# Optimization experiments

Hardware: AMD Instinct MI355X
Metric: run time of the kernel (lower is better)

The kernel has to match this reference:

```python
import jax, jax.numpy as jnp
import numpy as np

N_NODES = 150000
N_EDGES = 2400000
F_IN, HID, N_CLS = 22, 32, 6
BN_EPS = 1e-5


def setup_inputs() -> dict:
    key = jax.random.key(0)
    ks = jax.random.split(key, 10)
    x = jax.random.normal(ks[0], (N_NODES, F_IN), dtype=jnp.float32)
    edge_index = jax.random.randint(ks[1], (2, N_EDGES), 0, N_NODES, dtype=jnp.int64)
    # xavier-uniform style linear weights, zero biases (as in _init_weights)
    def xavier(k, fan_in, fan_out):
        lim = float(np.sqrt(6.0 / (fan_in + fan_out)))
        return jax.random.uniform(k, (fan_in, fan_out), jnp.float32, -lim, lim)
    return {
        "x": x,
        "edge_index": edge_index,
        "W_emb": xavier(ks[2], F_IN, HID),
        "b_emb": jnp.zeros((HID,), jnp.float32),
        "W_gcn": xavier(ks[3], HID, HID),
        "b_gcn": jnp.zeros((HID,), jnp.float32),
        "gamma": jnp.ones((HID,), jnp.float32),
        "beta": jnp.zeros((HID,), jnp.float32),
        "W_cls": xavier(ks[4], HID, N_CLS),
        "b_cls": jnp.zeros((N_CLS,), jnp.float32),
    }


def reference(x, edge_index, W_emb, b_emb, W_gcn, b_gcn, gamma, beta, W_cls, b_cls):
    N = x.shape[0]
    # embedding + relu
    h = jax.nn.relu(x @ W_emb + b_emb)                      # [N, HID]
    # GCNConv: linear transform first
    h = h @ W_gcn                                           # [N, HID]
    # add self-loops
    loops = jnp.arange(N, dtype=edge_index.dtype)
    src = jnp.concatenate([edge_index[0], loops])           # [E+N]
    dst = jnp.concatenate([edge_index[1], loops])
    # symmetric normalization deg^{-1/2} A_hat deg^{-1/2}
    deg = jax.ops.segment_sum(jnp.ones_like(dst, dtype=h.dtype), dst, num_segments=N)
    dis = jnp.where(deg > 0, jax.lax.rsqrt(jnp.where(deg > 0, deg, 1.0)), 0.0)
    norm = dis[src] * dis[dst]                              # [E+N]
    msg = h[src] * norm[:, None]                            # gather + scale
    agg = jax.ops.segment_sum(msg, dst, num_segments=N) + b_gcn
    # BatchNorm1d (training-mode batch statistics, biased variance)
    mean = jnp.mean(agg, axis=0)
    var = jnp.mean((agg - mean) ** 2, axis=0)
    hn = (agg - mean) * jax.lax.rsqrt(var + BN_EPS) * gamma + beta
    hn = jax.nn.relu(hn)
    # dropout is identity in eval; classifier
    return hn @ W_cls + b_cls
```

## Files before the change

kernel.cpp:

```cpp
#include <hip/hip_runtime.h>

#define N_NODES 150000
#define N_EDGES 2400000
#define F_IN    22
#define HID     32
#define N_CLS   6
#define BN_EPS  1e-5f

#define BSHIFT  8
#define BMASK   255
#define NB      ((N_NODES + BMASK) >> BSHIFT)
#define NBLK_BIN 256
#define CHUNK   ((N_EDGES + NBLK_BIN - 1) / NBLK_BIN)
#define CHUNK_H 8192
#define NBLK_H  ((N_EDGES + CHUNK_H - 1) / CHUNK_H)
#define NBLK_EMB ((N_NODES + 255) / 256)
#define NREP    8

__device__ __forceinline__ unsigned bf16rne(float f) {
    unsigned u = __float_as_uint(f);
    return (u + 0x7FFFu + ((u >> 16) & 1u)) >> 16;
}
__device__ __forceinline__ float bflo(unsigned p) { return __uint_as_float(p << 16); }
__device__ __forceinline__ float bfhi(unsigned p) { return __uint_as_float(p & 0xFFFF0000u); }

__global__ void embed_hist_kernel(const float* __restrict__ x,
                                  const float* __restrict__ W_emb,
                                  const float* __restrict__ b_emb,
                                  const float* __restrict__ W_gcn,
                                  unsigned* __restrict__ hb,
                                  const int* __restrict__ dst,
                                  int* __restrict__ bcnt) {
    if (blockIdx.x < NBLK_EMB) {
        __shared__ float sWe[F_IN * HID];
        __shared__ float sbe[HID];
        __shared__ float sWg[HID * HID];
        __shared__ unsigned sp[256 * 17];
        for (int t = threadIdx.x; t < F_IN * HID; t += blockDim.x) sWe[t] = W_emb[t];
        if (threadIdx.x < HID) sbe[threadIdx.x] = b_emb[threadIdx.x];
        for (int t = threadIdx.x; t < HID * HID; t += blockDim.x) sWg[t] = W_gcn[t];
        __syncthreads();

        int i = blockIdx.x * blockDim.x + threadIdx.x;
        bool act = i < N_NODES;

        if (act) {
            float xi[F_IN];
#pragma unroll
            for (int f = 0; f < F_IN; ++f) xi[f] = x[(size_t)i * F_IN + f];

            float h1[HID];
#pragma unroll
            for (int j = 0; j < HID; ++j) {
                float acc = sbe[j];
#pragma unroll
                for (int f = 0; f < F_IN; ++f) acc = fmaf(xi[f], sWe[f * HID + j], acc);
                h1[j] = fmaxf(acc, 0.0f);
            }
#pragma unroll
            for (int jj = 0; jj < HID / 2; ++jj) {
                float a0 = 0.0f, a1 = 0.0f;
#pragma unroll
                for (int f = 0; f < HID; ++f) {
                    a0 = fmaf(h1[f], sWg[f * HID + 2 * jj], a0);
                    a1 = fmaf(h1[f], sWg[f * HID + 2 * jj + 1], a1);
                }
                sp[threadIdx.x * 17 + jj] = bf16rne(a0) | (bf16rne(a1) << 16);
            }
        }
        __syncthreads();

        int nvalid = N_NODES - blockIdx.x * 256;
        if (nvalid > 256) nvalid = 256;
        int total = nvalid * 16;
        size_t gbase = (size_t)blockIdx.x * 256 * 16;
        for (int L = threadIdx.x; L < total; L += 256)
            hb[gbase + L] = sp[(L >> 4) * 17 + (L & 15)];
    } else {
        __shared__ int hloc[NB];
        for (int t = threadIdx.x; t < NB; t += 256) hloc[t] = 0;
        __syncthreads();
        int base = (blockIdx.x - NBLK_EMB) * CHUNK_H;
        int end = base + CHUNK_H; if (end > N_EDGES) end = N_EDGES;
        for (int i = base + threadIdx.x; i < end; i += 256)
            atomicAdd(&hloc[dst[i] >> BSHIFT], 1);
        __syncthreads();
        for (int t = threadIdx.x; t < NB; t += 256)
            if (hloc[t]) atomicAdd(&bcnt[t], hloc[t]);
    }
}

__global__ void bucket_scan_kernel(const int* __restrict__ bcnt,
                                   int* __restrict__ boff,
                                   int* __restrict__ bcur) {
    __shared__ int s[1024];
    int t = threadIdx.x;
    int v0 = (t < NB) ? bcnt[t] : 0;
    s[t] = v0;
    __syncthreads();
#pragma unroll
    for (int o = 1; o < 1024; o <<= 1) {
        int v = (t >= o) ? s[t - o] : 0;
        __syncthreads();
        s[t] += v;
        __syncthreads();
    }
    if (t < NB) {
        int e = s[t] - v0;
        boff[t] = e;
        bcur[t] = e;
    }
    if (t == NB - 1) boff[NB] = s[t];
}

__global__ void bin_edges_kernel(const int* __restrict__ src,
                                 const int* __restrict__ dst,
                                 int* __restrict__ bcur,
                                 unsigned int* __restrict__ binned) {
    __shared__ int hloc[NB];
    __shared__ int base[NB];
    __shared__ int lcur[NB];
    for (int t = threadIdx.x; t < NB; t += 512) hloc[t] = 0;
    __syncthreads();

    int cbase = blockIdx.x * CHUNK;
    int cend = cbase + CHUNK; if (cend > N_EDGES) cend = N_EDGES;
    for (int i = cbase + threadIdx.x; i < cend; i += 512)
        atomicAdd(&hloc[dst[i] >> BSHIFT], 1);
    __syncthreads();
    for (int t = threadIdx.x; t < NB; t += 512) {
        int c = hloc[t];
        base[t] = c ? atomicAdd(&bcur[t], c) : 0;
        lcur[t] = 0;
    }
    __syncthreads();
    for (int i = cbase + threadIdx.x; i < cend; i += 512) {
        int d = dst[i];
        int b = d >> BSHIFT;
        int r = atomicAdd(&lcur[b], 1);
        binned[base[b] + r] = ((unsigned)(d & BMASK) << 24) | (unsigned)src[i];
    }
}

__global__ void bucket_csr_kernel(const int* __restrict__ boff,
                                  const unsigned int* __restrict__ binned,
                                  int* __restrict__ sorted_src,
                                  int* __restrict__ off,
                                  float* __restrict__ dis) {
    __shared__ int s_cnt[256];
    __shared__ int s_scan[256];
    __shared__ int s_cur[256];
    int b = blockIdx.x;
    int t = threadIdx.x;
    int s0 = boff[b], s1 = boff[b + 1];
    int nbase = b << BSHIFT;
    int nnode = N_NODES - nbase; if (nnode > 256) nnode = 256;

    s_cnt[t] = 0;
    __syncthreads();
    for (int k = s0 + t; k < s1; k += 256)
        atomicAdd(&s_cnt[binned[k] >> 24], 1);
    __syncthreads();

    int v = s_cnt[t];
    s_scan[t] = v;
    __syncthreads();
#pragma unroll
    for (int o = 1; o < 256; o <<= 1) {
        int u = (t >= o) ? s_scan[t - o] : 0;
        __syncthreads();
        s_scan[t] += u;
        __syncthreads();
    }
    int excl = s_scan[t] - v;
    s_cur[t] = excl;
    if (t < nnode) {
        off[nbase + t] = s0 + excl;
        dis[nbase + t] = rsqrtf(1.0f + (float)v);
    }
    if (b == NB - 1 && t == 0) off[N_NODES] = N_EDGES;
    __syncthreads();

    for (int k = s0 + t; k < s1; k += 256) {
        unsigned p = binned[k];
        int n = (int)(p >> 24);
        int r = atomicAdd(&s_cur[n], 1);
        sorted_src[s0 + r] = (int)(p & 0xFFFFFFu);
    }
}

__global__ void aggregate_kernel(const int* __restrict__ off,
                                 const int* __restrict__ sorted_src,
                                 const unsigned* __restrict__ hb,
                                 const float* __restrict__ dis,
                                 float* __restrict__ agg,
                                 float* __restrict__ stats) {
    int t = blockIdx.x * blockDim.x + threadIdx.x;
    int node = t >> 3;
    int c = t & 7;
    bool active = node < N_NODES;

    float4 ps = {0.f, 0.f, 0.f, 0.f};
    float4 pq = {0.f, 0.f, 0.f, 0.f};

    if (active) {
        const uint2* hrow = reinterpret_cast<const uint2*>(hb);
        float dn = dis[node];
        uint2 hp = hrow[(size_t)node * 8 + c];
        float4 a0, a1, a2, a3;
        a0.x = bflo(hp.x) * dn; a0.y = bfhi(hp.x) * dn;
        a0.z = bflo(hp.y) * dn; a0.w = bfhi(hp.y) * dn;
        a1 = a2 = a3 = make_float4(0.f, 0.f, 0.f, 0.f);

        int b = off[node], e = off[node + 1];
        int k = b;
        for (; k + 8 <= e; k += 8) {
            int s0 = sorted_src[k],     s1 = sorted_src[k + 1];
            int s2 = sorted_src[k + 2], s3 = sorted_src[k + 3];
            int s4 = sorted_src[k + 4], s5 = sorted_src[k + 5];
            int s6 = sorted_src[k + 6], s7 = sorted_src[k + 7];
            float d0 = dis[s0], d1 = dis[s1], d2 = dis[s2], d3 = dis[s3];
            float d4 = dis[s4], d5 = dis[s5], d6 = dis[s6], d7 = dis[s7];
            uint2 v0 = hrow[(size_t)s0 * 8 + c];
            uint2 v1 = hrow[(size_t)s1 * 8 + c];
            uint2 v2 = hrow[(size_t)s2 * 8 + c];
            uint2 v3 = hrow[(size_t)s3 * 8 + c];
            uint2 v4 = hrow[(size_t)s4 * 8 + c];
            uint2 v5 = hrow[(size_t)s5 * 8 + c];
            uint2 v6 = hrow[(size_t)s6 * 8 + c];
            uint2 v7 = hrow[(size_t)s7 * 8 + c];
            a0.x = fmaf(bflo(v0.x), d0, a0.x); a0.y = fmaf(bfhi(v0.x), d0, a0.y);
            a0.z = fmaf(bflo(v0.y), d0, a0.z); a0.w = fmaf(bfhi(v0.y), d0, a0.w);
            a1.x = fmaf(bflo(v1.x), d1, a1.x); a1.y = fmaf(bfhi(v1.x), d1, a1.y);
            a1.z = fmaf(bflo(v1.y), d1, a1.z); a1.w = fmaf(bfhi(v1.y), d1, a1.w);
            a2.x = fmaf(bflo(v2.x), d2, a2.x); a2.y = fmaf(bfhi(v2.x), d2, a2.y);
            a2.z = fmaf(bflo(v2.y), d2, a2.z); a2.w = fmaf(bfhi(v2.y), d2, a2.w);
            a3.x = fmaf(bflo(v3.x), d3, a3.x); a3.y = fmaf(bfhi(v3.x), d3, a3.y);
            a3.z = fmaf(bflo(v3.y), d3, a3.z); a3.w = fmaf(bfhi(v3.y), d3, a3.w);
            a0.x = fmaf(bflo(v4.x), d4, a0.x); a0.y = fmaf(bfhi(v4.x), d4, a0.y);
            a0.z = fmaf(bflo(v4.y), d4, a0.z); a0.w = fmaf(bfhi(v4.y), d4, a0.w);
            a1.x = fmaf(bflo(v5.x), d5, a1.x); a1.y = fmaf(bfhi(v5.x), d5, a1.y);
            a1.z = fmaf(bflo(v5.y), d5, a1.z); a1.w = fmaf(bfhi(v5.y), d5, a1.w);
            a2.x = fmaf(bflo(v6.x), d6, a2.x); a2.y = fmaf(bfhi(v6.x), d6, a2.y);
            a2.z = fmaf(bflo(v6.y), d6, a2.z); a2.w = fmaf(bfhi(v6.y), d6, a2.w);
            a3.x = fmaf(bflo(v7.x), d7, a3.x); a3.y = fmaf(bfhi(v7.x), d7, a3.y);
            a3.z = fmaf(bflo(v7.y), d7, a3.z); a3.w = fmaf(bfhi(v7.y), d7, a3.w);
        }
        for (; k < e; ++k) {
            int s = sorted_src[k];
            float d = dis[s];
            uint2 v = hrow[(size_t)s * 8 + c];
            a0.x = fmaf(bflo(v.x), d, a0.x); a0.y = fmaf(bfhi(v.x), d, a0.y);
            a0.z = fmaf(bflo(v.y), d, a0.z); a0.w = fmaf(bfhi(v.y), d, a0.w);
        }
        float4 o;
        o.x = (a0.x + a1.x + a2.x + a3.x) * dn;
        o.y = (a0.y + a1.y + a2.y + a3.y) * dn;
        o.z = (a0.z + a1.z + a2.z + a3.z) * dn;
        o.w = (a0.w + a1.w + a2.w + a3.w) * dn;
        reinterpret_cast<float4*>(agg)[(size_t)node * 8 + c] = o;
        ps = o;
        pq.x = o.x * o.x; pq.y = o.y * o.y; pq.z = o.z * o.z; pq.w = o.w * o.w;
    }

    __shared__ float S[256 * 4];
    __shared__ float Q[256 * 4];
    S[threadIdx.x * 4 + 0] = ps.x; S[threadIdx.x * 4 + 1] = ps.y;
    S[threadIdx.x * 4 + 2] = ps.z; S[threadIdx.x * 4 + 3] = ps.w;
    Q[threadIdx.x * 4 + 0] = pq.x; Q[threadIdx.x * 4 + 1] = pq.y;
    Q[threadIdx.x * 4 + 2] = pq.z; Q[threadIdx.x * 4 + 3] = pq.w;
    __syncthreads();
    if (threadIdx.x < 32) {
        int cc = threadIdx.x >> 2, j = threadIdx.x & 3;
        float s = 0.0f, q = 0.0f;
#pragma unroll
        for (int w = 0; w < 32; ++w) {
            int tid = (w << 3) | cc;
            s += S[tid * 4 + j];
            q += Q[tid * 4 + j];
        }
        float* rep = stats + 64 * (blockIdx.x & (NREP - 1));
        atomicAdd(&rep[threadIdx.x], s);
        atomicAdd(&rep[32 + threadIdx.x], q);
    }
}

__global__ void cls_kernel(const float* __restrict__ agg,
                           const float* __restrict__ stats,
                           const float* __restrict__ gamma,
                           const float* __restrict__ beta,
                           const float* __restrict__ W_cls,
                           const float* __restrict__ b_cls,
                           float* __restrict__ out) {
    __shared__ float sA[HID];
    __shared__ float sB[HID];
    __shared__ float sW[HID * N_CLS];
    __shared__ float sb[N_CLS];
    if (threadIdx.x < HID) {
        float sum = 0.0f, sq = 0.0f;
#pragma unroll
        for (int r = 0; r < NREP; ++r) {
            sum += stats[r * 64 + threadIdx.x];
            sq  += stats[r * 64 + 32 + threadIdx.x];
        }
        const float invN = 1.0f / (float)N_NODES;
        float mean = sum * invN;
        float var = sq * invN - mean * mean;
        float inv = rsqrtf(var + BN_EPS);
        float A = gamma[threadIdx.x] * inv;
        sA[threadIdx.x] = A;
        sB[threadIdx.x] = beta[threadIdx.x] - mean * A;
    }
    for (int t = threadIdx.x; t < HID * N_CLS; t += blockDim.x) sW[t] = W_cls[t];
    if (threadIdx.x < N_CLS) sb[threadIdx.x] = b_cls[threadIdx.x];
    __syncthreads();

    int i = blockIdx.x * blockDim.x + threadIdx.x;
    if (i >= N_NODES) return;

    float acc[N_CLS];
#pragma unroll
    for (int c = 0; c < N_CLS; ++c) acc[c] = sb[c];
#pragma unroll
    for (int f = 0; f < HID; ++f) {
        float t = fmaxf(fmaf(agg[(size_t)i * HID + f], sA[f], sB[f]), 0.0f);
#pragma unroll
        for (int c = 0; c < N_CLS; ++c) acc[c] = fmaf(t, sW[f * N_CLS + c], acc[c]);
    }
#pragma unroll
    for (int c = 0; c < N_CLS; ++c) out[(size_t)i * N_CLS + c] = acc[c];
}

extern "C" void kernel_launch(void* const* d_in, const int* in_sizes, int n_in,
                              void* d_out, int out_size, void* d_ws, size_t ws_size,
                              hipStream_t stream) {
    const float* x     = (const float*)d_in[0];
    const int*   edge  = (const int*)d_in[1];
    const float* W_emb = (const float*)d_in[2];
    const float* b_emb = (const float*)d_in[3];
    const float* W_gcn = (const float*)d_in[4];
    const float* gamma = (const float*)d_in[6];
    const float* beta  = (const float*)d_in[7];
    const float* W_cls = (const float*)d_in[8];
    const float* b_cls = (const float*)d_in[9];
    float* out = (float*)d_out;

    unsigned*     hb         = (unsigned*)d_ws;
    float*        agg        = (float*)(hb + (size_t)N_NODES * HID / 2);
    float*        dis        = agg + (size_t)N_NODES * HID;
    int*          off        = (int*)(dis + N_NODES);
    int*          bcnt       = off + N_NODES + 1;
    int*          boff       = bcnt + NB;
    int*          bcur       = boff + NB + 1;
    unsigned int* binned     = (unsigned int*)(bcur + NB);
    int*          sorted_src = (int*)(binned + N_EDGES);
    float*        stats      = (float*)(sorted_src + N_EDGES);

    hipMemsetAsync(bcnt, 0, NB * sizeof(int), stream);
    hipMemsetAsync(stats, 0, 64 * NREP * sizeof(float), stream);

    const int* src = edge;
    const int* dst = edge + N_EDGES;

    embed_hist_kernel<<<NBLK_EMB + NBLK_H, 256, 0, stream>>>(x, W_emb, b_emb, W_gcn,
                                                             hb, dst, bcnt);
    bucket_scan_kernel<<<1, 1024, 0, stream>>>(bcnt, boff, bcur);
    bin_edges_kernel<<<NBLK_BIN, 512, 0, stream>>>(src, dst, bcur, binned);
    bucket_csr_kernel<<<NB, 256, 0, stream>>>(boff, binned, sorted_src, off, dis);
    aggregate_kernel<<<(N_NODES * 8 + 255) / 256, 256, 0, stream>>>(off, sorted_src,
                                                                    hb, dis, agg, stats);
    cls_kernel<<<(N_NODES + 255) / 256, 256, 0, stream>>>(agg, stats, gamma, beta,
                                                          W_cls, b_cls, out);
}
```

Measured before the change: 151.0 us.

## Move node embedding into the edge-binning launch and fold stats zeroing into scan

Splits the histogram into its own kernel and fuses the node embedding/GCN linear transform into the bin_edges launch as extra blocks of 512 threads. Embedding work now overlaps the scatter-heavy binning pass instead of the histogram pass. The stats memset is folded into the single-block scan kernel, which removes one API call. The shared-memory union is sized for the larger tile, which may reduce occupancy for the binning blocks.

```diff
diff --git a/kernel.cpp b/kernel.cpp
--- a/kernel.cpp
+++ b/kernel.cpp
@@ -14,7 +14,8 @@
 #define CHUNK   ((N_EDGES + NBLK_BIN - 1) / NBLK_BIN)
 #define CHUNK_H 8192
 #define NBLK_H  ((N_EDGES + CHUNK_H - 1) / CHUNK_H)
-#define NBLK_EMB ((N_NODES + 255) / 256)
+#define EMB_TILE 512
+#define NBLK_EMB ((N_NODES + EMB_TILE - 1) / EMB_TILE)
 #define NREP    8
 
 __device__ __forceinline__ unsigned bf16rne(float f) {
@@ -24,27 +25,96 @@
 __device__ __forceinline__ float bflo(unsigned p) { return __uint_as_float(p << 16); }
 __device__ __forceinline__ float bfhi(unsigned p) { return __uint_as_float(p & 0xFFFF0000u); }
 
-__global__ void embed_hist_kernel(const float* __restrict__ x,
-                                  const float* __restrict__ W_emb,
-                                  const float* __restrict__ b_emb,
-                                  const float* __restrict__ W_gcn,
-                                  unsigned* __restrict__ hb,
-                                  const int* __restrict__ dst,
-                                  int* __restrict__ bcnt) {
-    if (blockIdx.x < NBLK_EMB) {
-        __shared__ float sWe[F_IN * HID];
-        __shared__ float sbe[HID];
-        __shared__ float sWg[HID * HID];
-        __shared__ unsigned sp[256 * 17];
-        for (int t = threadIdx.x; t < F_IN * HID; t += blockDim.x) sWe[t] = W_emb[t];
+__global__ void hist_kernel(const int* __restrict__ dst,
+                            int* __restrict__ bcnt) {
+    __shared__ int hloc[NB];
+    for (int t = threadIdx.x; t < NB; t += 256) hloc[t] = 0;
+    __syncthreads();
+    int base = blockIdx.x * CHUNK_H;
+    int end = base + CHUNK_H; if (end > N_EDGES) end = N_EDGES;
+    for (int i = base + threadIdx.x; i < end; i += 256)
+        atomicAdd(&hloc[dst[i] >> BSHIFT], 1);
+    __syncthreads();
+    for (int t = threadIdx.x; t < NB; t += 256)
+        if (hloc[t]) atomicAdd(&bcnt[t], hloc[t]);
+}
+
+__global__ void bucket_scan_kernel(const int* __restrict__ bcnt,
+                                   int* __restrict__ boff,
+                                   int* __restrict__ bcur,
+                                   float* __restrict__ stats) {
+    int t = threadIdx.x;
+    if (t < 64 * NREP) stats[t] = 0.0f;
+    __shared__ int s[1024];
+    int v0 = (t < NB) ? bcnt[t] : 0;
+    s[t] = v0;
+    __syncthreads();
+#pragma unroll
+    for (int o = 1; o < 1024; o <<= 1) {
+        int v = (t >= o) ? s[t - o] : 0;
+        __syncthreads();
+        s[t] += v;
+        __syncthreads();
+    }
+    if (t < NB) {
+        int e = s[t] - v0;
+        boff[t] = e;
+        bcur[t] = e;
+    }
+    if (t == NB - 1) boff[NB] = s[t];
+}
+
+__global__ void bin_embed_kernel(const int* __restrict__ src,
+                                 const int* __restrict__ dst,
+                                 int* __restrict__ bcur,
+                                 unsigned int* __restrict__ binned,
+                                 const float* __restrict__ x,
+                                 const float* __restrict__ W_emb,
+                                 const float* __restrict__ b_emb,
+                                 const float* __restrict__ W_gcn,
+                                 unsigned* __restrict__ hb) {
+    __shared__ char smem[44672];
+    if (blockIdx.x < NBLK_BIN) {
+        int* hloc = (int*)smem;
+        int* base = hloc + NB;
+        int* lcur = base + NB;
+        for (int t = threadIdx.x; t < NB; t += 512) hloc[t] = 0;
+        __syncthreads();
+
+        int cbase = blockIdx.x * CHUNK;
+        int cend = cbase + CHUNK; if (cend > N_EDGES) cend = N_EDGES;
+        for (int i = cbase + threadIdx.x; i < cend; i += 512)
+            atomicAdd(&hloc[dst[i] >> BSHIFT], 1);
+        __syncthreads();
+        for (int t = threadIdx.x; t < NB; t += 512) {
+            int c = hloc[t];
+            base[t] = c ? atomicAdd(&bcur[t], c) : 0;
+            lcur[t] = 0;
+        }
+        __syncthreads();
+        for (int i = cbase + threadIdx.x; i < cend; i += 512) {
+            int d = dst[i];
+            int b = d >> BSHIFT;
+            int r = atomicAdd(&lcur[b], 1);
+            binned[base[b] + r] = ((unsigned)(d & BMASK) << 24) | (unsigned)src[i];
+        }
+    } else {
+        float* sWe = (float*)smem;
+        float* sbe = sWe + F_IN * HID;
+        float* sWg = sbe + HID;
+        unsigned* sp = (unsigned*)(sWg + HID * HID);
+        for (int t = threadIdx.x; t < F_IN * HID; t += 512) sWe[t] = W_emb[t];
         if (threadIdx.x < HID) sbe[threadIdx.x] = b_emb[threadIdx.x];
-        for (int t = threadIdx.x; t < HID * HID; t += blockDim.x) sWg[t] = W_gcn[t];
-        __syncthreads();
-
-        int i = blockIdx.x * blockDim.x + threadIdx.x;
-        bool act = i < N_NODES;
+        for (int t = threadIdx.x; t < HID * HID; t += 512) sWg[t] = W_gcn[t];
+        __syncthreads();
+
+        int eb = blockIdx.x - NBLK_BIN;
+        int nbase = eb * EMB_TILE;
+        int nvalid = N_NODES - nbase; if (nvalid > EMB_TILE) nvalid = EMB_TILE;
+        bool act = (int)threadIdx.x < nvalid;
 
         if (act) {
+            int i = nbase + threadIdx.x;
             float xi[F_IN];
 #pragma unroll
             for (int f = 0; f < F_IN; ++f) xi[f] = x[(size_t)i * F_IN + f];
@@ -70,75 +140,10 @@
         }
         __syncthreads();
 
-        int nvalid = N_NODES - blockIdx.x * 256;
-        if (nvalid > 256) nvalid = 256;
         int total = nvalid * 16;
-        size_t gbase = (size_t)blockIdx.x * 256 * 16;
-        for (int L = threadIdx.x; L < total; L += 256)
+        size_t gbase = (size_t)nbase * 16;
+        for (int L = threadIdx.x; L < total; L += 512)
             hb[gbase + L] = sp[(L >> 4) * 17 + (L & 15)];
-    } else {
-        __shared__ int hloc[NB];
-        for (int t = threadIdx.x; t < NB; t += 256) hloc[t] = 0;
-        __syncthreads();
-        int base = (blockIdx.x - NBLK_EMB) * CHUNK_H;
-        int end = base + CHUNK_H; if (end > N_EDGES) end = N_EDGES;
-        for (int i = base + threadIdx.x; i < end; i += 256)
-            atomicAdd(&hloc[dst[i] >> BSHIFT], 1);
-        __syncthreads();
-        for (int t = threadIdx.x; t < NB; t += 256)
-            if (hloc[t]) atomicAdd(&bcnt[t], hloc[t]);
-    }
-}
-
-__global__ void bucket_scan_kernel(const int* __restrict__ bcnt,
-                                   int* __restrict__ boff,
-                                   int* __restrict__ bcur) {
-    __shared__ int s[1024];
-    int t = threadIdx.x;
-    int v0 = (t < NB) ? bcnt[t] : 0;
-    s[t] = v0;
-    __syncthreads();
-#pragma unroll
-    for (int o = 1; o < 1024; o <<= 1) {
-        int v = (t >= o) ? s[t - o] : 0;
-        __syncthreads();
-        s[t] += v;
-        __syncthreads();
-    }
-    if (t < NB) {
-        int e = s[t] - v0;
-        boff[t] = e;
-        bcur[t] = e;
-    }
-    if (t == NB - 1) boff[NB] = s[t];
-}
-
-__global__ void bin_edges_kernel(const int* __restrict__ src,
-                                 const int* __restrict__ dst,
-                                 int* __restrict__ bcur,
-                                 unsigned int* __restrict__ binned) {
-    __shared__ int hloc[NB];
-    __shared__ int base[NB];
-    __shared__ int lcur[NB];
-    for (int t = threadIdx.x; t < NB; t += 512) hloc[t] = 0;
-    __syncthreads();
-
-    int cbase = blockIdx.x * CHUNK;
-    int cend = cbase + CHUNK; if (cend > N_EDGES) cend = N_EDGES;
-    for (int i = cbase + threadIdx.x; i < cend; i += 512)
-        atomicAdd(&hloc[dst[i] >> BSHIFT], 1);
-    __syncthreads();
-    for (int t = threadIdx.x; t < NB; t += 512) {
-        int c = hloc[t];
-        base[t] = c ? atomicAdd(&bcur[t], c) : 0;
-        lcur[t] = 0;
-    }
-    __syncthreads();
-    for (int i = cbase + threadIdx.x; i < cend; i += 512) {
-        int d = dst[i];
-        int b = d >> BSHIFT;
-        int r = atomicAdd(&lcur[b], 1);
-        binned[base[b] + r] = ((unsigned)(d & BMASK) << 24) | (unsigned)src[i];
     }
 }
 
@@ -357,15 +362,14 @@
     float*        stats      = (float*)(sorted_src + N_EDGES);
 
     hipMemsetAsync(bcnt, 0, NB * sizeof(int), stream);
-    hipMemsetAsync(stats, 0, 64 * NREP * sizeof(float), stream);
 
     const int* src = edge;
     const int* dst = edge + N_EDGES;
 
-    embed_hist_kernel<<<NBLK_EMB + NBLK_H, 256, 0, stream>>>(x, W_emb, b_emb, W_gcn,
-                                                             hb, dst, bcnt);
-    bucket_scan_kernel<<<1, 1024, 0, stream>>>(bcnt, boff, bcur);
-    bin_edges_kernel<<<NBLK_BIN, 512, 0, stream>>>(src, dst, bcur, binned);
+    hist_kernel<<<NBLK_H, 256, 0, stream>>>(dst, bcnt);
+    bucket_scan_kernel<<<1, 1024, 0, stream>>>(bcnt, boff, bcur, stats);
+    bin_embed_kernel<<<NBLK_BIN + NBLK_EMB, 512, 0, stream>>>(src, dst, bcur, binned,
+                                                              x, W_emb, b_emb, W_gcn, hb);
     bucket_csr_kernel<<<NB, 256, 0, stream>>>(boff, binned, sorted_src, off, dis);
     aggregate_kernel<<<(N_NODES * 8 + 255) / 256, 256, 0, stream>>>(off, sorted_src,
                                                                     hb, dis, agg, stats);
```

Result: slower. 246.6 us (+63.3%).
